# Kernel optimization log

Hardware: AMD Instinct MI355X
Metric: run time of the kernel (lower is better)

Reference implementation:

```python
import jax, jax.numpy as jnp
import numpy as np
from math import ceil

WIDTH, HEIGHT, NUM_TILE = 1920, 1080, 16
# NOTE: original code computes BOTH block dims from height (bug preserved for faithfulness)
BLOCK_W = ceil(HEIGHT / NUM_TILE)
BLOCK_H = ceil(HEIGHT / NUM_TILE)
T = NUM_TILE * NUM_TILE  # 256 tiles
N = 65536


def setup_inputs() -> dict:
    key = jax.random.key(0)
    k1, k2, k3 = jax.random.split(key, 3)
    pos2d = jax.random.uniform(k1, (N, 2), jnp.float32) * jnp.array([WIDTH, HEIGHT], jnp.float32)
    radius = jax.random.uniform(k2, (N,), jnp.float32) * 2.0  # radius in tile units, avg ~3x3 tile footprint
    depth = jax.random.uniform(k3, (N,), jnp.float32) * 10.0
    return {"pos2d": pos2d, "radius": radius, "depth": depth}


def _tile_binning(pos2d, radius, depth):
    minval, maxval = 0.0, NUM_TILE - 1e-5
    xmin = jnp.clip(pos2d[:, 0] / BLOCK_W - radius, minval, maxval).astype(jnp.int32)
    xmax = jnp.clip(pos2d[:, 0] / BLOCK_W + radius, minval, maxval).astype(jnp.int32)
    ymin = jnp.clip(pos2d[:, 1] / BLOCK_H - radius, minval, maxval).astype(jnp.int32)
    ymax = jnp.clip(pos2d[:, 1] / BLOCK_H + radius, minval, maxval).astype(jnp.int32)

    tr = jnp.arange(NUM_TILE, dtype=jnp.int32)
    in_x = (tr[None, :] >= xmin[:, None]) & (tr[None, :] <= xmax[:, None])  # [N, 16]
    in_y = (tr[None, :] >= ymin[:, None]) & (tr[None, :] <= ymax[:, None])  # [N, 16]
    # tile index t = xi + NUM_TILE * yi  -> mask[n, yi, xi]
    mask = (in_y[:, :, None] & in_x[:, None, :]).reshape(N, T)  # [N, T]

    # inclusive-cumsum bucket offsets (matches torch.cumsum(tile_count))
    tile_count = jnp.cumsum(mask.sum(axis=0).astype(jnp.int32)).astype(jnp.int32)  # [T]
    total = tile_count[-1]

    # flattened entry list, tile-major then primitive-index order (matches scatter loop order)
    maskT = mask.T.reshape(-1)                                   # [T*N]
    tile_id = jnp.repeat(jnp.arange(T, dtype=jnp.int32), N)      # [T*N]
    prim_id = jnp.tile(jnp.arange(N, dtype=jnp.int32), T)        # [T*N]
    depth_e = depth[prim_id]
    tile_eff = jnp.where(maskT, tile_id, T)  # invalid entries pushed past all real tiles

    # segmented depth sort: primary key tile, secondary depth, tertiary prim (stable tiebreak)
    order = jnp.lexsort((prim_id, depth_e, tile_eff))
    prim_sorted = prim_id[order]
    valid = jnp.arange(T * N) < total
    tile_indices = jnp.where(valid, prim_sorted, -1).astype(jnp.int32)  # [T*N], -1 padded
    return tile_count, tile_indices


def reference(pos2d, radius, depth):
    # Equivalent of Screen.create_tiles(pos2d, radius) followed by Screen.depth_sort(depth).
    # Returns (tile_count: inclusive cumsum bucket offsets [T],
    #          tile_indices: per-tile depth-sorted primitive ids, padded to T*N with -1).
    return _tile_binning(pos2d, radius, depth)
```

## Files before the change

### kernel.cpp

```cpp
#include <hip/hip_runtime.h>
#include <stdint.h>

#define NPRIM 65536
#define NT 16
#define T_TILES 256
#define NBKT 2048
#define BCAP 256
#define NBLK 64
#define CTHR 512
#define CBLK 512
#define FILLB (CBLK - T_TILES)

typedef unsigned long long u64;
typedef unsigned int u32;

__device__ __forceinline__ u32 dbucket(float d) {
    u32 b = (u32)(d * 204.8f);
    return b > (NBKT - 1) ? (NBKT - 1) : b;
}

__global__ __launch_bounds__(256) void k_compute(
    const float2* __restrict__ pos2d, const float* __restrict__ radius,
    const float* __restrict__ depth, u64* __restrict__ keysRaw,
    u32* __restrict__ bounds, u32* __restrict__ counts_blk,
    u32* __restrict__ bh)
{
    __shared__ u32 hist[T_TILES];
    __shared__ u32 bhist[NBKT];
    int tid = threadIdx.x;
    hist[tid] = 0;
    for (int j = tid; j < NBKT; j += 256) bhist[j] = 0;
    __syncthreads();

    int base = blockIdx.x * 1024;
    const float mx = (float)(16.0 - 1e-5);
    #pragma unroll
    for (int q = 0; q < 4; ++q) {
        int i = base + q * 256 + tid;
        float2 p = pos2d[i];
        float r = radius[i];
        float fx = p.x / 68.0f;
        float fy = p.y / 68.0f;
        int xmin = (int)fminf(fmaxf(fx - r, 0.0f), mx);
        int xmax = (int)fminf(fmaxf(fx + r, 0.0f), mx);
        int ymin = (int)fminf(fmaxf(fy - r, 0.0f), mx);
        int ymax = (int)fminf(fmaxf(fy + r, 0.0f), mx);
        bounds[i] = (u32)(xmin | (xmax << 4) | (ymin << 8) | (ymax << 12));
        float d = depth[i];
        u32 lrank = atomicAdd(&bhist[dbucket(d)], 1u);
        keysRaw[i] = ((u64)lrank << 48) | ((u64)__float_as_uint(d) << 16) | (u32)i;
        for (int ty = ymin; ty <= ymax; ++ty)
            for (int tx = xmin; tx <= xmax; ++tx)
                atomicAdd(&hist[ty * NT + tx], 1u);
    }
    __syncthreads();
    counts_blk[blockIdx.x * 256 + tid] = hist[tid];
    for (int j = tid; j < NBKT; j += 256) bh[blockIdx.x * NBKT + j] = bhist[j];
}

__global__ __launch_bounds__(256) void k_scatter(
    const u64* __restrict__ keysRaw, const u32* __restrict__ bh,
    u64* __restrict__ keysBkt, u32* __restrict__ bucket_base,
    u32* __restrict__ bucket_count)
{
    __shared__ u32 loff[NBKT];
    __shared__ u32 wsum[4];
    int tid = threadIdx.x, lane = tid & 63, wave = tid >> 6;
    int blk = blockIdx.x;

    u32 c8[8] = {0,0,0,0,0,0,0,0};
    u32 p8[8] = {0,0,0,0,0,0,0,0};
    for (int b = 0; b < NBLK; ++b) {
        const uint4* row = (const uint4*)(bh + b * NBKT + tid * 8);
        uint4 h0 = row[0], h1 = row[1];
        u32 h[8] = {h0.x, h0.y, h0.z, h0.w, h1.x, h1.y, h1.z, h1.w};
        #pragma unroll
        for (int j = 0; j < 8; ++j) {
            if (b < blk) p8[j] += h[j];
            c8[j] += h[j];
        }
    }
    u32 sum8 = 0;
    #pragma unroll
    for (int j = 0; j < 8; ++j) sum8 += c8[j];
    u32 v = sum8;
    #pragma unroll
    for (int d = 1; d < 64; d <<= 1) {
        u32 t = __shfl_up(v, d, 64);
        if (lane >= d) v += t;
    }
    if (lane == 63) wsum[wave] = v;
    __syncthreads();
    u32 add = 0;
    for (int w = 0; w < wave; ++w) add += wsum[w];
    u32 run = v + add - sum8;
    #pragma unroll
    for (int j = 0; j < 8; ++j) {
        loff[tid * 8 + j] = run + p8[j];
        if (blk == 0) {
            bucket_base[tid * 8 + j] = run;
            bucket_count[tid * 8 + j] = c8[j];
        }
        run += c8[j];
    }
    __syncthreads();

    int base = blk * 1024;
    #pragma unroll
    for (int q = 0; q < 4; ++q) {
        u64 key = keysRaw[base + q * 256 + tid];
        u32 d = dbucket(__uint_as_float((u32)(key >> 16)));
        u32 lrank = (u32)(key >> 48);
        keysBkt[loff[d] + lrank] = key & 0x0000FFFFFFFFFFFFull;
    }
}

__global__ __launch_bounds__(256) void k_bsort(
    const u64* __restrict__ keysBkt, const u32* __restrict__ bucket_base,
    const u32* __restrict__ bucket_count, const u32* __restrict__ bounds,
    u32* __restrict__ entries)
{
    __shared__ u64 buf[4][BCAP];
    int tid = threadIdx.x, lane = tid & 63, wave = tid >> 6;
    int bucket = blockIdx.x * 4 + wave;
    u32 base = bucket_base[bucket];
    u32 n = bucket_count[bucket];
    if (n > BCAP) n = BCAP;
    #pragma unroll
    for (int t = 0; t < 4; ++t) {
        u32 i = (u32)lane + 64u * t;
        if (i < n) buf[wave][i] = keysBkt[base + i];
    }
    __syncthreads();
    #pragma unroll
    for (int t = 0; t < 4; ++t) {
        u32 i = (u32)lane + 64u * t;
        if (i < n) {
            u64 ki = buf[wave][i];
            u32 r = 0;
            for (u32 j = 0; j < n; ++j) r += (buf[wave][j] < ki);
            u32 prim = (u32)ki & 0xFFFFu;
            entries[base + r] = (bounds[prim] << 16) | prim;
        }
    }
}

__global__ __launch_bounds__(CTHR) void k_compact(
    const uint4* __restrict__ entries4, const u32* __restrict__ counts_blk,
    int* __restrict__ tile_count, int* __restrict__ out_idx)
{
    __shared__ u32 cnt[T_TILES];
    __shared__ u32 excl[T_TILES];
    __shared__ u32 wsum[4];
    __shared__ u32 chunkcnt[64];
    __shared__ u32 chunkoff[64];
    int b = blockIdx.x, tid = threadIdx.x, lane = tid & 63, wave = tid >> 6;

    if (tid < 256) {
        u32 s = 0;
        for (int bb = 0; bb < NBLK; ++bb) s += counts_blk[bb * 256 + tid];
        cnt[tid] = s;
    }
    __syncthreads();
    if (tid < 256) {
        u32 c = cnt[tid], v = c;
        #pragma unroll
        for (int d = 1; d < 64; d <<= 1) {
            u32 t = __shfl_up(v, d, 64);
            if (lane >= d) v += t;
        }
        if (lane == 63) wsum[wave] = v;
        excl[tid] = v;
    }
    __syncthreads();
    if (tid < 256) {
        u32 add = 0;
        for (int w = 0; w < wave; ++w) add += wsum[w];
        u32 incl = excl[tid] + add;
        excl[tid] = incl - cnt[tid];
        cnt[tid] = incl;
        if (b == 0) tile_count[tid] = (int)incl;
    }
    __syncthreads();
    u32 total = cnt[T_TILES - 1];

    if (b >= T_TILES) {
        const u32 end = (u32)T_TILES * (u32)NPRIM;
        u32 s4 = (total + 3u) & ~3u;
        if (b == T_TILES && tid < (int)(s4 - total)) out_idx[total + tid] = -1;
        u32 n4 = (end - s4) >> 2;
        int4* o4 = (int4*)(out_idx + s4);
        int4 m1 = make_int4(-1, -1, -1, -1);
        u32 gid = (u32)(b - T_TILES) * (u32)CTHR + (u32)tid;
        for (u32 i = gid; i < n4; i += (u32)FILLB * (u32)CTHR) o4[i] = m1;
        return;
    }

    int tile = b, tx = tile & 15, ty = tile >> 4;
    u32 base0 = excl[tile];
    u64 lmask = (1ull << lane) - 1;

    for (int cc = 0; cc < 8; ++cc) {
        int ch = wave * 8 + cc;
        u32 cs = 0;
        #pragma unroll
        for (int k = 0; k < 4; ++k) {
            uint4 e = entries4[ch * 256 + k * 64 + lane];
            u32 ev[4] = {e.x, e.y, e.z, e.w};
            #pragma unroll
            for (int q = 0; q < 4; ++q) {
                u32 bb2 = ev[q] >> 16;
                bool m = (tx >= (int)(bb2 & 15)) && (tx <= (int)((bb2 >> 4) & 15))
                      && (ty >= (int)((bb2 >> 8) & 15)) && (ty <= (int)((bb2 >> 12) & 15));
                cs += (u32)__popcll(__ballot(m));
            }
        }
        if (lane == 0) chunkcnt[ch] = cs;
    }
    __syncthreads();
    if (tid < 64) {
        u32 c2 = chunkcnt[tid], v2 = c2;
        #pragma unroll
        for (int d = 1; d < 64; d <<= 1) {
            u32 t = __shfl_up(v2, d, 64);
            if (lane >= d) v2 += t;
        }
        chunkoff[tid] = base0 + v2 - c2;
    }
    __syncthreads();

    for (int cc = 0; cc < 8; ++cc) {
        int ch = wave * 8 + cc;
        u32 run = chunkoff[ch];
        #pragma unroll
        for (int k = 0; k < 4; ++k) {
            uint4 e = entries4[ch * 256 + k * 64 + lane];
            u32 ev[4] = {e.x, e.y, e.z, e.w};
            bool m[4]; u64 bal[4];
            #pragma unroll
            for (int q = 0; q < 4; ++q) {
                u32 bb2 = ev[q] >> 16;
                m[q] = (tx >= (int)(bb2 & 15)) && (tx <= (int)((bb2 >> 4) & 15))
                    && (ty >= (int)((bb2 >> 8) & 15)) && (ty <= (int)((bb2 >> 12) & 15));
                bal[q] = __ballot(m[q]);
            }
            u32 pre = (u32)(__popcll(bal[0] & lmask) + __popcll(bal[1] & lmask)
                          + __popcll(bal[2] & lmask) + __popcll(bal[3] & lmask));
            #pragma unroll
            for (int q = 0; q < 4; ++q) {
                if (m[q]) { out_idx[run + pre] = (int)(ev[q] & 0xFFFFu); pre++; }
            }
            run += (u32)(__popcll(bal[0]) + __popcll(bal[1])
                       + __popcll(bal[2]) + __popcll(bal[3]));
        }
    }
}

extern "C" void kernel_launch(void* const* d_in, const int* in_sizes, int n_in,
                              void* d_out, int out_size, void* d_ws, size_t ws_size,
                              hipStream_t stream)
{
    const float2* pos2d  = (const float2*)d_in[0];
    const float*  radius = (const float*)d_in[1];
    const float*  depth  = (const float*)d_in[2];

    int* out32        = (int*)d_out;
    int* tile_count   = out32;
    int* tile_indices = out32 + T_TILES;

    char* ws = (char*)d_ws;
    u64* keysRaw      = (u64*)(ws);
    u64* keysBkt      = (u64*)(ws + 512 * 1024);
    u32* bounds       = (u32*)(ws + 1024 * 1024);
    u32* counts_blk   = (u32*)(ws + 1280 * 1024);
    u32* bh           = (u32*)(ws + 1344 * 1024);
    u32* bucket_base  = (u32*)(ws + 1856 * 1024);
    u32* bucket_count = (u32*)(ws + 1864 * 1024);

    k_compute<<<NBLK, 256, 0, stream>>>(pos2d, radius, depth, keysRaw, bounds,
                                        counts_blk, bh);
    k_scatter<<<NBLK, 256, 0, stream>>>(keysRaw, bh, keysBkt,
                                        bucket_base, bucket_count);

    u32* entries = (u32*)keysRaw;
    k_bsort<<<NBKT / 4, 256, 0, stream>>>(keysBkt, bucket_base, bucket_count,
                                          bounds, entries);
    k_compact<<<CBLK, CTHR, 0, stream>>>((const uint4*)entries, counts_blk,
                                         tile_count, tile_indices);
}
```

Before: 145.5 us.

## Move tile prefix scan into scatter and replace -1 fill with memset

The per-tile count reduction and scan now run once in an extra block of k_scatter, which writes tile_count and exclusive offsets to workspace. Previously every k_compact block redid this work. The -1 padding of the 64 MB output moves from 256 extra compact blocks to a hipMemsetAsync over the whole output issued before the pipeline. The memset writes the full buffer, including the region later overwritten, so it adds write traffic but frees compact of the fill blocks and the redundant scan.

```diff
diff --git a/kernel.cpp b/kernel.cpp
--- a/kernel.cpp
+++ b/kernel.cpp
@@ -8,8 +8,6 @@
 #define BCAP 256
 #define NBLK 64
 #define CTHR 512
-#define CBLK 512
-#define FILLB (CBLK - T_TILES)
 
 typedef unsigned long long u64;
 typedef unsigned int u32;
@@ -61,13 +59,33 @@
 __global__ __launch_bounds__(256) void k_scatter(
     const u64* __restrict__ keysRaw, const u32* __restrict__ bh,
     u64* __restrict__ keysBkt, u32* __restrict__ bucket_base,
-    u32* __restrict__ bucket_count)
-{
-    __shared__ u32 loff[NBKT];
+    u32* __restrict__ bucket_count, const u32* __restrict__ counts_blk,
+    int* __restrict__ tile_count, u32* __restrict__ excl_off)
+{
     __shared__ u32 wsum[4];
     int tid = threadIdx.x, lane = tid & 63, wave = tid >> 6;
     int blk = blockIdx.x;
 
+    if (blk == NBLK) {
+        u32 s = 0;
+        for (int bb = 0; bb < NBLK; ++bb) s += counts_blk[bb * 256 + tid];
+        u32 v = s;
+        #pragma unroll
+        for (int d = 1; d < 64; d <<= 1) {
+            u32 t = __shfl_up(v, d, 64);
+            if (lane >= d) v += t;
+        }
+        if (lane == 63) wsum[wave] = v;
+        __syncthreads();
+        u32 add = 0;
+        for (int w = 0; w < wave; ++w) add += wsum[w];
+        u32 incl = v + add;
+        tile_count[tid] = (int)incl;
+        excl_off[tid] = incl - s;
+        return;
+    }
+
+    __shared__ u32 loff[NBKT];
     u32 c8[8] = {0,0,0,0,0,0,0,0};
     u32 p8[8] = {0,0,0,0,0,0,0,0};
     for (int b = 0; b < NBLK; ++b) {
@@ -146,58 +164,14 @@
 }
 
 __global__ __launch_bounds__(CTHR) void k_compact(
-    const uint4* __restrict__ entries4, const u32* __restrict__ counts_blk,
-    int* __restrict__ tile_count, int* __restrict__ out_idx)
-{
-    __shared__ u32 cnt[T_TILES];
-    __shared__ u32 excl[T_TILES];
-    __shared__ u32 wsum[4];
+    const uint4* __restrict__ entries4, const u32* __restrict__ excl_off,
+    int* __restrict__ out_idx)
+{
     __shared__ u32 chunkcnt[64];
     __shared__ u32 chunkoff[64];
-    int b = blockIdx.x, tid = threadIdx.x, lane = tid & 63, wave = tid >> 6;
-
-    if (tid < 256) {
-        u32 s = 0;
-        for (int bb = 0; bb < NBLK; ++bb) s += counts_blk[bb * 256 + tid];
-        cnt[tid] = s;
-    }
-    __syncthreads();
-    if (tid < 256) {
-        u32 c = cnt[tid], v = c;
-        #pragma unroll
-        for (int d = 1; d < 64; d <<= 1) {
-            u32 t = __shfl_up(v, d, 64);
-            if (lane >= d) v += t;
-        }
-        if (lane == 63) wsum[wave] = v;
-        excl[tid] = v;
-    }
-    __syncthreads();
-    if (tid < 256) {
-        u32 add = 0;
-        for (int w = 0; w < wave; ++w) add += wsum[w];
-        u32 incl = excl[tid] + add;
-        excl[tid] = incl - cnt[tid];
-        cnt[tid] = incl;
-        if (b == 0) tile_count[tid] = (int)incl;
-    }
-    __syncthreads();
-    u32 total = cnt[T_TILES - 1];
-
-    if (b >= T_TILES) {
-        const u32 end = (u32)T_TILES * (u32)NPRIM;
-        u32 s4 = (total + 3u) & ~3u;
-        if (b == T_TILES && tid < (int)(s4 - total)) out_idx[total + tid] = -1;
-        u32 n4 = (end - s4) >> 2;
-        int4* o4 = (int4*)(out_idx + s4);
-        int4 m1 = make_int4(-1, -1, -1, -1);
-        u32 gid = (u32)(b - T_TILES) * (u32)CTHR + (u32)tid;
-        for (u32 i = gid; i < n4; i += (u32)FILLB * (u32)CTHR) o4[i] = m1;
-        return;
-    }
-
-    int tile = b, tx = tile & 15, ty = tile >> 4;
-    u32 base0 = excl[tile];
+    int tile = blockIdx.x, tid = threadIdx.x, lane = tid & 63, wave = tid >> 6;
+    int tx = tile & 15, ty = tile >> 4;
+    u32 base0 = excl_off[tile];
     u64 lmask = (1ull << lane) - 1;
 
     for (int cc = 0; cc < 8; ++cc) {
@@ -276,15 +250,19 @@
     u32* bh           = (u32*)(ws + 1344 * 1024);
     u32* bucket_base  = (u32*)(ws + 1856 * 1024);
     u32* bucket_count = (u32*)(ws + 1864 * 1024);
+    u32* excl_off     = (u32*)(ws + 1872 * 1024);
+
+    (void)hipMemsetAsync(tile_indices, 0xFF, (size_t)T_TILES * NPRIM * 4, stream);
 
     k_compute<<<NBLK, 256, 0, stream>>>(pos2d, radius, depth, keysRaw, bounds,
                                         counts_blk, bh);
-    k_scatter<<<NBLK, 256, 0, stream>>>(keysRaw, bh, keysBkt,
-                                        bucket_base, bucket_count);
+    k_scatter<<<NBLK + 1, 256, 0, stream>>>(keysRaw, bh, keysBkt,
+                                            bucket_base, bucket_count,
+                                            counts_blk, tile_count, excl_off);
 
     u32* entries = (u32*)keysRaw;
     k_bsort<<<NBKT / 4, 256, 0, stream>>>(keysBkt, bucket_base, bucket_count,
                                           bounds, entries);
-    k_compact<<<CBLK, CTHR, 0, stream>>>((const uint4*)entries, counts_blk,
-                                         tile_count, tile_indices);
-}
+    k_compact<<<T_TILES, CTHR, 0, stream>>>((const uint4*)entries, excl_off,
+                                            tile_indices);
+}
```

After: 150.1 us. 1.03x slower.
